# Performance work log

Measured on AMD Instinct MI355X. Metric: run time of the kernel, lower is better.

## Reference

```python
import jax, jax.numpy as jnp
import numpy as np

EPS = 1e-5  # torch GroupNorm default


def setup_inputs() -> dict:
    key = jax.random.key(0)
    k1, k2, k3 = jax.random.split(key, 3)
    bs, l, dim = 16, 2048, 512
    G, varDim, numCodes = 2, 256, 320
    x = jax.random.normal(k1, (bs, l, dim), dtype=jnp.float32)
    # grouped 1x1 Conv1d weight: (groups, out_per_group, in_per_group)
    proj_w = jax.random.normal(k2, (G, varDim, varDim), dtype=jnp.float32) / np.sqrt(varDim)
    gn_weight = jnp.ones((dim,), dtype=jnp.float32)
    gn_bias = jnp.zeros((dim,), dtype=jnp.float32)
    embeddings = 0.01 * jax.random.normal(k3, (numCodes, 1, varDim), dtype=jnp.float32)
    return {"x": x, "proj_w": proj_w, "gn_weight": gn_weight,
            "gn_bias": gn_bias, "embeddings": embeddings}


def reference(x, proj_w, gn_weight, gn_bias, embeddings):
    bs, l, dim = x.shape
    G, varDim, _ = proj_w.shape
    numCodes = embeddings.shape[0]

    # --- projection: grouped 1x1 conv ---
    xg = x.transpose(0, 2, 1).reshape(bs, G, varDim, l)            # (bs,G,v,l)
    ze_g = jnp.einsum('gov,bgvl->bgol', proj_w, xg)                # (bs,G,v,l)

    # --- Fp32GroupNorm over (C/G * L) per group ---
    zf = ze_g.astype(jnp.float32)
    mean = zf.mean(axis=(2, 3), keepdims=True)
    var = zf.var(axis=(2, 3), keepdims=True)
    zn = (zf - mean) * jax.lax.rsqrt(var + EPS)
    ze = zn.reshape(bs, dim, l) * gn_weight[None, :, None] + gn_bias[None, :, None]
    ze = ze.astype(x.dtype)                                        # (bs,dim,l)

    # --- VQ: nearest code per group (argmin of L2 == argmin of sq dist) ---
    z = ze.reshape(bs, G, varDim, l).transpose(0, 3, 1, 2)         # (bs,l,G,v)
    emb = jnp.broadcast_to(embeddings, (numCodes, G, varDim))      # combineGroups expand
    dots = jnp.einsum('blgv,cgv->blgc', z, emb)                    # (bs,l,G,C)
    e2 = jnp.sum(emb * emb, axis=-1)                               # (C,G)
    dist = e2.T[None, None] - 2.0 * dots                           # ||z||^2 dropped: const over C
    idx = jnp.argmin(dist, axis=-1)                                # (bs,l,G)

    # gather codes per group
    zq = jnp.take_along_axis(
        emb.transpose(1, 0, 2)[None, None],                        # (1,1,G,C,v)
        idx[..., None, None], axis=3).squeeze(3)                   # (bs,l,G,v)
    zq = zq.reshape(bs, l, dim)

    # straight-through estimator; output shape (bs, l, dim)
    ze_bld = ze.transpose(0, 2, 1)
    out = jax.lax.stop_gradient(zq) + ze_bld - jax.lax.stop_gradient(ze_bld)
    return out
```

## Files before the change

### kernel.cpp

```cpp
#include <hip/hip_runtime.h>
#include <math.h>

typedef _Float16 half8_t  __attribute__((ext_vector_type(8)));
typedef _Float16 half4_t  __attribute__((ext_vector_type(4)));
typedef float    floatx16 __attribute__((ext_vector_type(16)));

#define BS   16
#define LL   2048
#define DIMC 512
#define NG   2
#define VD   256
#define NC   320
#define NELEM ((double)(VD*LL))

__global__ void k_prep(const float* __restrict__ W, const float* __restrict__ emb,
                       _Float16* __restrict__ Whg, _Float16* __restrict__ Wlg,
                       _Float16* __restrict__ Ehg, _Float16* __restrict__ Elg)
{
  int id = blockIdx.x * 256 + threadIdx.x;
  if (id < NG * VD * VD) {
    float w = W[id] * 16.0f;
    _Float16 h = (_Float16)w;
    Whg[id] = h;
    Wlg[id] = (_Float16)(w - (float)h);
  } else {
    int j = id - NG * VD * VD;
    if (j < NC * VD) {
      float e = emb[j] * 64.0f;
      _Float16 h = (_Float16)e;
      Ehg[j] = h;
      Elg[j] = (_Float16)(e - (float)h);
    }
  }
}

__global__ __launch_bounds__(256, 2) void k_proj(
    const float* __restrict__ x,
    const _Float16* __restrict__ Whg, const _Float16* __restrict__ Wlg,
    float* __restrict__ ze, double* __restrict__ stats)
{
  __shared__ _Float16 Ah[128][72];
  __shared__ _Float16 Bh[128][72];

  const int blk = blockIdx.x;
  const int g  = blk & 1;
  const int nb = (blk >> 1) & 1;
  const int mt = blk >> 2;
  const int m0 = mt * 128;
  const int n0 = nb * 128;
  const int b  = m0 >> 11;
  const int t  = threadIdx.x;
  const int lane = t & 63;
  const int w    = t >> 6;
  const int col  = lane & 31;
  const int hq   = lane >> 5;
  const int mw   = (w & 1) * 64;
  const int nw   = (w >> 1) * 64;

  floatx16 acc[2][2];
  #pragma unroll
  for (int i = 0; i < 2; ++i)
    #pragma unroll
    for (int j = 0; j < 2; ++j)
      #pragma unroll
      for (int e = 0; e < 16; ++e) acc[i][j][e] = 0.f;

  for (int k0 = 0; k0 < VD; k0 += 32) {
    #pragma unroll
    for (int i = 0; i < 4; ++i) {
      int idx = i * 256 + t;
      int row = idx >> 3, kq = idx & 7;
      float4 v = *(const float4*)(x + ((size_t)(m0 + row)) * DIMC + g * VD + k0 + kq * 4);
      half4_t hh, ll;
      { _Float16 h = (_Float16)v.x; hh[0] = h; ll[0] = (_Float16)(v.x - (float)h); }
      { _Float16 h = (_Float16)v.y; hh[1] = h; ll[1] = (_Float16)(v.y - (float)h); }
      { _Float16 h = (_Float16)v.z; hh[2] = h; ll[2] = (_Float16)(v.z - (float)h); }
      { _Float16 h = (_Float16)v.w; hh[3] = h; ll[3] = (_Float16)(v.w - (float)h); }
      *(half4_t*)&Ah[row][kq * 4]      = hh;
      *(half4_t*)&Ah[row][32 + kq * 4] = ll;
    }
    #pragma unroll
    for (int i = 0; i < 2; ++i) {
      int idx = i * 256 + t;
      int row = idx >> 2, kc = idx & 3;
      size_t off = ((size_t)(g * VD + n0 + row)) * VD + k0 + kc * 8;
      *(half8_t*)&Bh[row][kc * 8]      = *(const half8_t*)(Whg + off);
      *(half8_t*)&Bh[row][32 + kc * 8] = *(const half8_t*)(Wlg + off);
    }
    __syncthreads();
    #pragma unroll
    for (int ks = 0; ks < 2; ++ks) {
      const int ko = ks * 16 + hq * 8;
      half8_t azh[2], azl[2], bwh[2], bwl[2];
      #pragma unroll
      for (int i2 = 0; i2 < 2; ++i2) {
        azh[i2] = *(const half8_t*)&Ah[mw + i2 * 32 + col][ko];
        azl[i2] = *(const half8_t*)&Ah[mw + i2 * 32 + col][32 + ko];
        bwh[i2] = *(const half8_t*)&Bh[nw + i2 * 32 + col][ko];
        bwl[i2] = *(const half8_t*)&Bh[nw + i2 * 32 + col][32 + ko];
      }
      #pragma unroll
      for (int mi = 0; mi < 2; ++mi)
        #pragma unroll
        for (int ni = 0; ni < 2; ++ni) {
          acc[mi][ni] = __builtin_amdgcn_mfma_f32_32x32x16_f16(azh[mi], bwh[ni], acc[mi][ni], 0, 0, 0);
          acc[mi][ni] = __builtin_amdgcn_mfma_f32_32x32x16_f16(azh[mi], bwl[ni], acc[mi][ni], 0, 0, 0);
          acc[mi][ni] = __builtin_amdgcn_mfma_f32_32x32x16_f16(azl[mi], bwh[ni], acc[mi][ni], 0, 0, 0);
        }
    }
    __syncthreads();
  }

  double s1 = 0.0, s2 = 0.0;
  #pragma unroll
  for (int mi = 0; mi < 2; ++mi)
    #pragma unroll
    for (int ni = 0; ni < 2; ++ni)
      #pragma unroll
      for (int r = 0; r < 16; ++r) {
        float vv = acc[mi][ni][r] * 0.0625f;
        double d = (double)vv; s1 += d; s2 += d * d;
        int ml = mw + mi * 32 + (r & 3) + 8 * (r >> 2) + 4 * hq;
        int nl = nw + ni * 32 + col;
        ze[((size_t)(m0 + ml)) * DIMC + g * VD + n0 + nl] = vv;
      }
  #pragma unroll
  for (int off = 32; off > 0; off >>= 1) {
    s1 += __shfl_down(s1, off);
    s2 += __shfl_down(s2, off);
  }
  if (lane == 0) {
    atomicAdd(&stats[(b * NG + g) * 2 + 0], s1);
    atomicAdd(&stats[(b * NG + g) * 2 + 1], s2);
  }
}

__global__ void k_fin(const double* __restrict__ stats,
                      const float* __restrict__ emb,
                      float* __restrict__ msr, float* __restrict__ e2f)
{
  const int t = threadIdx.x;
  if (blockIdx.x == 0) {
    if (t < BS * NG) {
      double s1 = stats[2 * t], s2 = stats[2 * t + 1];
      double mean = s1 / NELEM;
      double var  = s2 / NELEM - mean * mean;
      double rstd = 1.0 / sqrt(var + 1e-5);
      msr[t]      = (float)mean;
      msr[32 + t] = (float)rstd;
    }
  } else {
    const int c = (blockIdx.x - 1) * 64 + t;
    const float* er = emb + (size_t)c * VD;
    double s[4] = {0.0, 0.0, 0.0, 0.0};
    #pragma unroll
    for (int v = 0; v < VD; v += 16) {
      #pragma unroll
      for (int u = 0; u < 4; ++u) {
        float4 e4 = *(const float4*)(er + v + u * 4);
        s[u] += (double)e4.x * e4.x + (double)e4.y * e4.y
              + (double)e4.z * e4.z + (double)e4.w * e4.w;
      }
    }
    e2f[c] = (float)(64.0 * (s[0] + s[1] + s[2] + s[3]));
  }
}

__global__ __launch_bounds__(256, 2) void k_vq(
    float* __restrict__ zio, const float* __restrict__ emb,
    const _Float16* __restrict__ Ehg, const _Float16* __restrict__ Elg,
    const float* __restrict__ gnw, const float* __restrict__ gnb,
    const float* __restrict__ msr, const float* __restrict__ e2f)
{
  __shared__ _Float16 Ah[64][72];
  __shared__ _Float16 Es[320][72];
  __shared__ float e2sh[NC];
  __shared__ int idxs[64];

  const int blk = blockIdx.x;
  const int g  = blk & 1;
  const int m0 = (blk >> 1) * 64;
  const int b  = m0 >> 11;
  const int t  = threadIdx.x;
  const int lane = t & 63;
  const int w    = t >> 6;
  const int col  = lane & 31;
  const int hq   = lane >> 5;
  const int mhalf = w & 1;
  const int nhalf = w >> 1;
  const int ml = mhalf * 32 + col;

  const float mean = msr[b * NG + g];
  const float rstd = msr[32 + b * NG + g];
  for (int c = t; c < NC; c += 256) e2sh[c] = e2f[c];

  float* zbase = zio + ((size_t)m0) * DIMC + g * VD;
  const float* gw = gnw + g * VD;
  const float* gb = gnb + g * VD;

  floatx16 acc[5];
  #pragma unroll
  for (int i = 0; i < 5; ++i)
    #pragma unroll
    for (int e = 0; e < 16; ++e) acc[i][e] = 0.f;

  for (int k0 = 0; k0 < VD; k0 += 32) {
    #pragma unroll
    for (int i = 0; i < 2; ++i) {
      int idx = i * 256 + t;
      int row = idx >> 3, kq = idx & 7;
      float4 v  = *(const float4*)(zbase + ((size_t)row) * DIMC + k0 + kq * 4);
      float4 w4 = *(const float4*)(gw + k0 + kq * 4);
      float4 b4 = *(const float4*)(gb + k0 + kq * 4);
      float zn0 = (v.x - mean) * rstd * w4.x + b4.x;
      float zn1 = (v.y - mean) * rstd * w4.y + b4.y;
      float zn2 = (v.z - mean) * rstd * w4.z + b4.z;
      float zn3 = (v.w - mean) * rstd * w4.w + b4.w;
      half4_t hh, ll;
      { _Float16 h = (_Float16)zn0; hh[0] = h; ll[0] = (_Float16)(zn0 - (float)h); }
      { _Float16 h = (_Float16)zn1; hh[1] = h; ll[1] = (_Float16)(zn1 - (float)h); }
      { _Float16 h = (_Float16)zn2; hh[2] = h; ll[2] = (_Float16)(zn2 - (float)h); }
      { _Float16 h = (_Float16)zn3; hh[3] = h; ll[3] = (_Float16)(zn3 - (float)h); }
      *(half4_t*)&Ah[row][kq * 4]      = hh;
      *(half4_t*)&Ah[row][32 + kq * 4] = ll;
    }
    #pragma unroll
    for (int i = 0; i < 5; ++i) {
      int idx = i * 256 + t;
      int row = idx >> 2, kc = idx & 3;
      size_t off = ((size_t)row) * VD + k0 + kc * 8;
      *(half8_t*)&Es[row][kc * 8]      = *(const half8_t*)(Ehg + off);
      *(half8_t*)&Es[row][32 + kc * 8] = *(const half8_t*)(Elg + off);
    }
    __syncthreads();
    #pragma unroll
    for (int ks = 0; ks < 2; ++ks) {
      const int ko = ks * 16 + hq * 8;
      half8_t azh = *(const half8_t*)&Ah[ml][ko];
      half8_t azl = *(const half8_t*)&Ah[ml][32 + ko];
      #pragma unroll
      for (int nt = 0; nt < 5; ++nt) {
        int nr = nhalf * 160 + nt * 32 + col;
        half8_t beh = *(const half8_t*)&Es[nr][ko];
        half8_t bel = *(const half8_t*)&Es[nr][32 + ko];
        acc[nt] = __builtin_amdgcn_mfma_f32_32x32x16_f16(azh, beh, acc[nt], 0, 0, 0);
        acc[nt] = __builtin_amdgcn_mfma_f32_32x32x16_f16(azh, bel, acc[nt], 0, 0, 0);
        acc[nt] = __builtin_amdgcn_mfma_f32_32x32x16_f16(azl, beh, acc[nt], 0, 0, 0);
      }
    }
    __syncthreads();
  }

  float* bestv = (float*)&Es[0][0];
  int*   besti = (int*)((char*)&Es[0][0] + 64 * 65 * 4);
  #pragma unroll
  for (int r = 0; r < 16; ++r) {
    int mloc = mhalf * 32 + (r & 3) + 8 * (r >> 2) + 4 * hq;
    float bv = 3.4e38f; int bn = 0;
    #pragma unroll
    for (int nt = 0; nt < 5; ++nt) {
      int n = nhalf * 160 + nt * 32 + col;
      float d = e2sh[n] - 2.0f * acc[nt][r];
      if (d < bv) { bv = d; bn = n; }
    }
    bestv[mloc * 65 + nhalf * 32 + col] = bv;
    besti[mloc * 65 + nhalf * 32 + col] = bn;
  }
  __syncthreads();
  if (t < 64) {
    float bv = bestv[t * 65]; int bn = besti[t * 65];
    for (int j = 1; j < 64; ++j) {
      float v = bestv[t * 65 + j]; int n = besti[t * 65 + j];
      if (v < bv || (v == bv && n < bn)) { bv = v; bn = n; }
    }
    idxs[t] = bn;
  }
  __syncthreads();

  #pragma unroll
  for (int it = 0; it < 16; ++it) {
    int idx = it * 256 + t;
    int row = idx >> 6, q4 = (idx & 63) * 4;
    int id = idxs[row];
    float4 zr = *(const float4*)(zbase + (size_t)row * DIMC + q4);
    float4 w4 = *(const float4*)(gw + q4);
    float4 b4 = *(const float4*)(gb + q4);
    float4 e4 = *(const float4*)(emb + (size_t)id * VD + q4);
    float4 o; float zn;
    zn = (zr.x - mean) * rstd * w4.x + b4.x; o.x = (e4.x + zn) - zn;
    zn = (zr.y - mean) * rstd * w4.y + b4.y; o.y = (e4.y + zn) - zn;
    zn = (zr.z - mean) * rstd * w4.z + b4.z; o.z = (e4.z + zn) - zn;
    zn = (zr.w - mean) * rstd * w4.w + b4.w; o.w = (e4.w + zn) - zn;
    *(float4*)(zbase + (size_t)row * DIMC + q4) = o;
  }
}

extern "C" void kernel_launch(void* const* d_in, const int* in_sizes, int n_in,
                              void* d_out, int out_size, void* d_ws, size_t ws_size,
                              hipStream_t stream) {
  const float* x   = (const float*)d_in[0];
  const float* W   = (const float*)d_in[1];
  const float* gnw = (const float*)d_in[2];
  const float* gnb = (const float*)d_in[3];
  const float* emb = (const float*)d_in[4];
  float* out = (float*)d_out;

  double*   stats = (double*)d_ws;
  float*    msr   = (float*)((char*)d_ws + 512);
  float*    e2f   = (float*)((char*)d_ws + 768);
  _Float16* Whg   = (_Float16*)((char*)d_ws + 4096);
  _Float16* Wlg   = (_Float16*)((char*)d_ws + 266240);
  _Float16* Ehg   = (_Float16*)((char*)d_ws + 528384);
  _Float16* Elg   = (_Float16*)((char*)d_ws + 692224);

  hipMemsetAsync(d_ws, 0, 512, stream);
  k_prep<<<(NG * VD * VD + NC * VD + 255) / 256, 256, 0, stream>>>(W, emb, Whg, Wlg, Ehg, Elg);
  k_proj<<<1024, 256, 0, stream>>>(x, Whg, Wlg, out, stats);
  k_fin<<<6, 64, 0, stream>>>(stats, emb, msr, e2f);
  k_vq<<<1024, 256, 0, stream>>>(out, emb, Ehg, Elg, gnw, gnb, msr, e2f);
}
```

Before: 231.7 us.

## Widen GEMM tiles, prebuild LDS images, direct global-to-LDS loads, fold finalize kernel

```diff
diff --git a/kernel.cpp b/kernel.cpp
--- a/kernel.cpp
+++ b/kernel.cpp
@@ -13,64 +13,84 @@
 #define NC   320
 #define NELEM ((double)(VD*LL))
 
+#define GLL(gsrc, ldst) __builtin_amdgcn_global_load_lds( \
+    (const __attribute__((address_space(1))) unsigned int*)(gsrc), \
+    (__attribute__((address_space(3))) unsigned int*)(ldst), 16, 0, 0)
+
 __global__ void k_prep(const float* __restrict__ W, const float* __restrict__ emb,
-                       _Float16* __restrict__ Whg, _Float16* __restrict__ Wlg,
-                       _Float16* __restrict__ Ehg, _Float16* __restrict__ Elg)
+                       _Float16* __restrict__ Wimg, _Float16* __restrict__ Eimg,
+                       float* __restrict__ e2f, double* __restrict__ stats)
 {
-  int id = blockIdx.x * 256 + threadIdx.x;
-  if (id < NG * VD * VD) {
+  const int blk = blockIdx.x, t = threadIdx.x;
+  if (blk < 512) {
+    int id = blk * 256 + t;
+    int k = id & 255, c = k >> 5, kk = k & 31;
+    int row = (id >> 8) & 255, g = id >> 16;
     float w = W[id] * 16.0f;
     _Float16 h = (_Float16)w;
-    Whg[id] = h;
-    Wlg[id] = (_Float16)(w - (float)h);
+    size_t base = ((size_t)(g * 8 + c) * 256 + row) * 72;
+    Wimg[base + kk]      = h;
+    Wimg[base + 32 + kk] = (_Float16)(w - (float)h);
+  } else if (blk < 832) {
+    int j = (blk - 512) * 256 + t;
+    int k = j & 255, c = k >> 5, kk = k & 31;
+    int code = j >> 8;
+    float e = emb[j] * 64.0f;
+    _Float16 h = (_Float16)e;
+    size_t base = ((size_t)c * 320 + code) * 72;
+    Eimg[base + kk]      = h;
+    Eimg[base + 32 + kk] = (_Float16)(e - (float)h);
+  } else if (blk < 834) {
+    int code = (blk - 832) * 256 + t;
+    if (code < NC) {
+      const float* er = emb + (size_t)code * VD;
+      double s[4] = {0.0, 0.0, 0.0, 0.0};
+      for (int v = 0; v < VD; v += 16)
+        #pragma unroll
+        for (int u = 0; u < 4; ++u) {
+          float4 e4 = *(const float4*)(er + v + u * 4);
+          s[u] += (double)e4.x * e4.x + (double)e4.y * e4.y
+                + (double)e4.z * e4.z + (double)e4.w * e4.w;
+        }
+      e2f[code] = (float)(64.0 * (s[0] + s[1] + s[2] + s[3]));
+    }
   } else {
-    int j = id - NG * VD * VD;
-    if (j < NC * VD) {
-      float e = emb[j] * 64.0f;
-      _Float16 h = (_Float16)e;
-      Ehg[j] = h;
-      Elg[j] = (_Float16)(e - (float)h);
-    }
+    if (t < 64) stats[t] = 0.0;
   }
 }
 
 __global__ __launch_bounds__(256, 2) void k_proj(
-    const float* __restrict__ x,
-    const _Float16* __restrict__ Whg, const _Float16* __restrict__ Wlg,
+    const float* __restrict__ x, const _Float16* __restrict__ Wimg,
     float* __restrict__ ze, double* __restrict__ stats)
 {
   __shared__ _Float16 Ah[128][72];
-  __shared__ _Float16 Bh[128][72];
+  __shared__ _Float16 Bh[256 * 72];
 
   const int blk = blockIdx.x;
   const int g  = blk & 1;
-  const int nb = (blk >> 1) & 1;
-  const int mt = blk >> 2;
-  const int m0 = mt * 128;
-  const int n0 = nb * 128;
+  const int m0 = (blk >> 1) * 128;
   const int b  = m0 >> 11;
   const int t  = threadIdx.x;
-  const int lane = t & 63;
-  const int w    = t >> 6;
-  const int col  = lane & 31;
-  const int hq   = lane >> 5;
-  const int mw   = (w & 1) * 64;
-  const int nw   = (w >> 1) * 64;
-
-  floatx16 acc[2][2];
+  const int lane = t & 63, w = t >> 6;
+  const int col  = lane & 31, hq = lane >> 5;
+  const int mw = (w & 1) * 64, nw = (w >> 1) * 128;
+
+  const char* wbase = (const char*)(Wimg + (size_t)g * 8 * 256 * 72);
+
+  floatx16 acc[2][4];
   #pragma unroll
   for (int i = 0; i < 2; ++i)
     #pragma unroll
-    for (int j = 0; j < 2; ++j)
+    for (int j = 0; j < 4; ++j)
       #pragma unroll
       for (int e = 0; e < 16; ++e) acc[i][j][e] = 0.f;
 
-  for (int k0 = 0; k0 < VD; k0 += 32) {
+  for (int c = 0; c < 8; ++c) {
     #pragma unroll
     for (int i = 0; i < 4; ++i) {
       int idx = i * 256 + t;
       int row = idx >> 3, kq = idx & 7;
-      float4 v = *(const float4*)(x + ((size_t)(m0 + row)) * DIMC + g * VD + k0 + kq * 4);
+      float4 v = *(const float4*)(x + ((size_t)(m0 + row)) * DIMC + g * VD + c * 32 + kq * 4);
       half4_t hh, ll;
       { _Float16 h = (_Float16)v.x; hh[0] = h; ll[0] = (_Float16)(v.x - (float)h); }
       { _Float16 h = (_Float16)v.y; hh[1] = h; ll[1] = (_Float16)(v.y - (float)h); }
@@ -79,30 +99,33 @@
       *(half4_t*)&Ah[row][kq * 4]      = hh;
       *(half4_t*)&Ah[row][32 + kq * 4] = ll;
     }
-    #pragma unroll
-    for (int i = 0; i < 2; ++i) {
-      int idx = i * 256 + t;
-      int row = idx >> 2, kc = idx & 3;
-      size_t off = ((size_t)(g * VD + n0 + row)) * VD + k0 + kc * 8;
-      *(half8_t*)&Bh[row][kc * 8]      = *(const half8_t*)(Whg + off);
-      *(half8_t*)&Bh[row][32 + kc * 8] = *(const half8_t*)(Wlg + off);
+    {
+      const char* wc = wbase + (size_t)c * 256 * 144;
+      #pragma unroll
+      for (int i = 0; i < 9; ++i) {
+        int off = (w * 9 + i) * 1024 + lane * 16;
+        GLL(wc + off, (char*)Bh + off);
+      }
     }
     __syncthreads();
     #pragma unroll
     for (int ks = 0; ks < 2; ++ks) {
       const int ko = ks * 16 + hq * 8;
-      half8_t azh[2], azl[2], bwh[2], bwl[2];
-      #pragma unroll
-      for (int i2 = 0; i2 < 2; ++i2) {
-        azh[i2] = *(const half8_t*)&Ah[mw + i2 * 32 + col][ko];
-        azl[i2] = *(const half8_t*)&Ah[mw + i2 * 32 + col][32 + ko];
-        bwh[i2] = *(const half8_t*)&Bh[nw + i2 * 32 + col][ko];
-        bwl[i2] = *(const half8_t*)&Bh[nw + i2 * 32 + col][32 + ko];
+      half8_t azh[2], azl[2], bwh[4], bwl[4];
+      #pragma unroll
+      for (int i = 0; i < 2; ++i) {
+        azh[i] = *(const half8_t*)&Ah[mw + i * 32 + col][ko];
+        azl[i] = *(const half8_t*)&Ah[mw + i * 32 + col][32 + ko];
+      }
+      #pragma unroll
+      for (int j = 0; j < 4; ++j) {
+        bwh[j] = *(const half8_t*)&Bh[(nw + j * 32 + col) * 72 + ko];
+        bwl[j] = *(const half8_t*)&Bh[(nw + j * 32 + col) * 72 + 32 + ko];
       }
       #pragma unroll
       for (int mi = 0; mi < 2; ++mi)
         #pragma unroll
-        for (int ni = 0; ni < 2; ++ni) {
+        for (int ni = 0; ni < 4; ++ni) {
           acc[mi][ni] = __builtin_amdgcn_mfma_f32_32x32x16_f16(azh[mi], bwh[ni], acc[mi][ni], 0, 0, 0);
           acc[mi][ni] = __builtin_amdgcn_mfma_f32_32x32x16_f16(azh[mi], bwl[ni], acc[mi][ni], 0, 0, 0);
           acc[mi][ni] = __builtin_amdgcn_mfma_f32_32x32x16_f16(azl[mi], bwh[ni], acc[mi][ni], 0, 0, 0);
@@ -115,14 +138,14 @@
   #pragma unroll
   for (int mi = 0; mi < 2; ++mi)
     #pragma unroll
-    for (int ni = 0; ni < 2; ++ni)
+    for (int ni = 0; ni < 4; ++ni)
       #pragma unroll
       for (int r = 0; r < 16; ++r) {
         float vv = acc[mi][ni][r] * 0.0625f;
         double d = (double)vv; s1 += d; s2 += d * d;
         int ml = mw + mi * 32 + (r & 3) + 8 * (r >> 2) + 4 * hq;
         int nl = nw + ni * 32 + col;
-        ze[((size_t)(m0 + ml)) * DIMC + g * VD + n0 + nl] = vv;
+        ze[((size_t)(m0 + ml)) * DIMC + g * VD + nl] = vv;
       }
   #pragma unroll
   for (int off = 32; off > 0; off >>= 1) {
@@ -135,83 +158,51 @@
   }
 }
 
-__global__ void k_fin(const double* __restrict__ stats,
-                      const float* __restrict__ emb,
-                      float* __restrict__ msr, float* __restrict__ e2f)
-{
-  const int t = threadIdx.x;
-  if (blockIdx.x == 0) {
-    if (t < BS * NG) {
-      double s1 = stats[2 * t], s2 = stats[2 * t + 1];
-      double mean = s1 / NELEM;
-      double var  = s2 / NELEM - mean * mean;
-      double rstd = 1.0 / sqrt(var + 1e-5);
-      msr[t]      = (float)mean;
-      msr[32 + t] = (float)rstd;
-    }
-  } else {
-    const int c = (blockIdx.x - 1) * 64 + t;
-    const float* er = emb + (size_t)c * VD;
-    double s[4] = {0.0, 0.0, 0.0, 0.0};
-    #pragma unroll
-    for (int v = 0; v < VD; v += 16) {
-      #pragma unroll
-      for (int u = 0; u < 4; ++u) {
-        float4 e4 = *(const float4*)(er + v + u * 4);
-        s[u] += (double)e4.x * e4.x + (double)e4.y * e4.y
-              + (double)e4.z * e4.z + (double)e4.w * e4.w;
-      }
-    }
-    e2f[c] = (float)(64.0 * (s[0] + s[1] + s[2] + s[3]));
-  }
-}
-
 __global__ __launch_bounds__(256, 2) void k_vq(
     float* __restrict__ zio, const float* __restrict__ emb,
-    const _Float16* __restrict__ Ehg, const _Float16* __restrict__ Elg,
+    const _Float16* __restrict__ Eimg,
     const float* __restrict__ gnw, const float* __restrict__ gnb,
-    const float* __restrict__ msr, const float* __restrict__ e2f)
+    const double* __restrict__ stats, const float* __restrict__ e2f)
 {
-  __shared__ _Float16 Ah[64][72];
-  __shared__ _Float16 Es[320][72];
+  __shared__ _Float16 Zs[128][72];
+  __shared__ _Float16 Es[320 * 72];
   __shared__ float e2sh[NC];
-  __shared__ int idxs[64];
+  __shared__ int idxs[128];
 
   const int blk = blockIdx.x;
   const int g  = blk & 1;
-  const int m0 = (blk >> 1) * 64;
+  const int m0 = (blk >> 1) * 128;
   const int b  = m0 >> 11;
   const int t  = threadIdx.x;
-  const int lane = t & 63;
-  const int w    = t >> 6;
-  const int col  = lane & 31;
-  const int hq   = lane >> 5;
-  const int mhalf = w & 1;
-  const int nhalf = w >> 1;
-  const int ml = mhalf * 32 + col;
-
-  const float mean = msr[b * NG + g];
-  const float rstd = msr[32 + b * NG + g];
+  const int lane = t & 63, w = t >> 6;
+  const int col  = lane & 31, hq = lane >> 5;
+
+  const int si = b * NG + g;
+  double ss1 = stats[2 * si], ss2 = stats[2 * si + 1];
+  double mu = ss1 / NELEM, var = ss2 / NELEM - mu * mu;
+  const float mean = (float)mu;
+  const float rstd = (float)(1.0 / sqrt(var + 1e-5));
+
   for (int c = t; c < NC; c += 256) e2sh[c] = e2f[c];
 
-  float* zbase = zio + ((size_t)m0) * DIMC + g * VD;
+  float* zbase = zio + (size_t)m0 * DIMC + g * VD;
   const float* gw = gnw + g * VD;
   const float* gb = gnb + g * VD;
 
-  floatx16 acc[5];
-  #pragma unroll
-  for (int i = 0; i < 5; ++i)
+  floatx16 acc[10];
+  #pragma unroll
+  for (int i = 0; i < 10; ++i)
     #pragma unroll
     for (int e = 0; e < 16; ++e) acc[i][e] = 0.f;
 
-  for (int k0 = 0; k0 < VD; k0 += 32) {
-    #pragma unroll
-    for (int i = 0; i < 2; ++i) {
+  for (int c = 0; c < 8; ++c) {
+    #pragma unroll
+    for (int i = 0; i < 4; ++i) {
       int idx = i * 256 + t;
       int row = idx >> 3, kq = idx & 7;
-      float4 v  = *(const float4*)(zbase + ((size_t)row) * DIMC + k0 + kq * 4);
-      float4 w4 = *(const float4*)(gw + k0 + kq * 4);
-      float4 b4 = *(const float4*)(gb + k0 + kq * 4);
+      float4 v  = *(const float4*)(zbase + (size_t)row * DIMC + c * 32 + kq * 4);
+      float4 w4 = *(const float4*)(gw + c * 32 + kq * 4);
+      float4 b4 = *(const float4*)(gb + c * 32 + kq * 4);
       float zn0 = (v.x - mean) * rstd * w4.x + b4.x;
       float zn1 = (v.y - mean) * rstd * w4.y + b4.y;
       float zn2 = (v.z - mean) * rstd * w4.z + b4.z;
@@ -221,64 +212,53 @@
       { _Float16 h = (_Float16)zn1; hh[1] = h; ll[1] = (_Float16)(zn1 - (float)h); }
       { _Float16 h = (_Float16)zn2; hh[2] = h; ll[2] = (_Float16)(zn2 - (float)h); }
       { _Float16 h = (_Float16)zn3; hh[3] = h; ll[3] = (_Float16)(zn3 - (float)h); }
-      *(half4_t*)&Ah[row][kq * 4]      = hh;
-      *(half4_t*)&Ah[row][32 + kq * 4] = ll;
-    }
-    #pragma unroll
-    for (int i = 0; i < 5; ++i) {
-      int idx = i * 256 + t;
-      int row = idx >> 2, kc = idx & 3;
-      size_t off = ((size_t)row) * VD + k0 + kc * 8;
-      *(half8_t*)&Es[row][kc * 8]      = *(const half8_t*)(Ehg + off);
-      *(half8_t*)&Es[row][32 + kc * 8] = *(const half8_t*)(Elg + off);
+      *(half4_t*)&Zs[row][kq * 4]      = hh;
+      *(half4_t*)&Zs[row][32 + kq * 4] = ll;
+    }
+    {
+      const char* ec = (const char*)Eimg + (size_t)c * 320 * 144;
+      for (int i = w; i < 45; i += 4) {
+        int off = i * 1024 + lane * 16;
+        GLL(ec + off, (char*)Es + off);
+      }
     }
     __syncthreads();
     #pragma unroll
     for (int ks = 0; ks < 2; ++ks) {
       const int ko = ks * 16 + hq * 8;
-      half8_t azh = *(const half8_t*)&Ah[ml][ko];
-      half8_t azl = *(const half8_t*)&Ah[ml][32 + ko];
-      #pragma unroll
-      for (int nt = 0; nt < 5; ++nt) {
-        int nr = nhalf * 160 + nt * 32 + col;
-        half8_t beh = *(const half8_t*)&Es[nr][ko];
-        half8_t bel = *(const half8_t*)&Es[nr][32 + ko];
-        acc[nt] = __builtin_amdgcn_mfma_f32_32x32x16_f16(azh, beh, acc[nt], 0, 0, 0);
-        acc[nt] = __builtin_amdgcn_mfma_f32_32x32x16_f16(azh, bel, acc[nt], 0, 0, 0);
-        acc[nt] = __builtin_amdgcn_mfma_f32_32x32x16_f16(azl, beh, acc[nt], 0, 0, 0);
-      }
-    }
-    __syncthreads();
-  }
-
-  float* bestv = (float*)&Es[0][0];
-  int*   besti = (int*)((char*)&Es[0][0] + 64 * 65 * 4);
-  #pragma unroll
-  for (int r = 0; r < 16; ++r) {
-    int mloc = mhalf * 32 + (r & 3) + 8 * (r >> 2) + 4 * hq;
-    float bv = 3.4e38f; int bn = 0;
-    #pragma unroll
-    for (int nt = 0; nt < 5; ++nt) {
-      int n = nhalf * 160 + nt * 32 + col;
-      float d = e2sh[n] - 2.0f * acc[nt][r];
-      if (d < bv) { bv = d; bn = n; }
-    }
-    bestv[mloc * 65 + nhalf * 32 + col] = bv;
-    besti[mloc * 65 + nhalf * 32 + col] = bn;
-  }
+      half8_t bzh = *(const half8_t*)&Zs[w * 32 + col][ko];
+      half8_t bzl = *(const half8_t*)&Zs[w * 32 + col][32 + ko];
+      #pragma unroll
+      for (int mt = 0; mt < 10; ++mt) {
+        half8_t aeh = *(const half8_t*)&Es[(mt * 32 + col) * 72 + ko];
+        half8_t ael = *(const half8_t*)&Es[(mt * 32 + col) * 72 + 32 + ko];
+        acc[mt] = __builtin_amdgcn_mfma_f32_32x32x16_f16(aeh, bzh, acc[mt], 0, 0, 0);
+        acc[mt] = __builtin_amdgcn_mfma_f32_32x32x16_f16(aeh, bzl, acc[mt], 0, 0, 0);
+        acc[mt] = __builtin_amdgcn_mfma_f32_32x32x16_f16(ael, bzh, acc[mt], 0, 0, 0);
+      }
+    }
+    __syncthreads();
+  }
+
+  float bv = 3.4e38f; int bi = 0x7fffffff;
+  #pragma unroll
+  for (int mt = 0; mt < 10; ++mt)
+    #pragma unroll
+    for (int r = 0; r < 16; ++r) {
+      int code = mt * 32 + (r & 3) + 8 * (r >> 2) + 4 * hq;
+      float d = e2sh[code] - 2.0f * acc[mt][r];
+      if (d < bv || (d == bv && code < bi)) { bv = d; bi = code; }
+    }
+  {
+    float ov = __shfl_xor(bv, 32);
+    int   oi = __shfl_xor(bi, 32);
+    if (ov < bv || (ov == bv && oi < bi)) { bv = ov; bi = oi; }
+  }
+  if (hq == 0) idxs[w * 32 + col] = bi;
   __syncthreads();
-  if (t < 64) {
-    float bv = bestv[t * 65]; int bn = besti[t * 65];
-    for (int j = 1; j < 64; ++j) {
-      float v = bestv[t * 65 + j]; int n = besti[t * 65 + j];
-      if (v < bv || (v == bv && n < bn)) { bv = v; bn = n; }
-    }
-    idxs[t] = bn;
-  }
-  __syncthreads();
-
-  #pragma unroll
-  for (int it = 0; it < 16; ++it) {
+
+  #pragma unroll
+  for (int it = 0; it < 32; ++it) {
     int idx = it * 256 + t;
     int row = idx >> 6, q4 = (idx & 63) * 4;
     int id = idxs[row];
@@ -306,16 +286,11 @@
   float* out = (float*)d_out;
 
   double*   stats = (double*)d_ws;
-  float*    msr   = (float*)((char*)d_ws + 512);
-  float*    e2f   = (float*)((char*)d_ws + 768);
-  _Float16* Whg   = (_Float16*)((char*)d_ws + 4096);
-  _Float16* Wlg   = (_Float16*)((char*)d_ws + 266240);
-  _Float16* Ehg   = (_Float16*)((char*)d_ws + 528384);
-  _Float16* Elg   = (_Float16*)((char*)d_ws + 692224);
-
-  hipMemsetAsync(d_ws, 0, 512, stream);
-  k_prep<<<(NG * VD * VD + NC * VD + 255) / 256, 256, 0, stream>>>(W, emb, Whg, Wlg, Ehg, Elg);
-  k_proj<<<1024, 256, 0, stream>>>(x, Whg, Wlg, out, stats);
-  k_fin<<<6, 64, 0, stream>>>(stats, emb, msr, e2f);
-  k_vq<<<1024, 256, 0, stream>>>(out, emb, Ehg, Elg, gnw, gnb, msr, e2f);
-}
+  float*    e2f   = (float*)((char*)d_ws + 512);
+  _Float16* Wimg  = (_Float16*)((char*)d_ws + 2048);
+  _Float16* Eimg  = (_Float16*)((char*)d_ws + 591872);
+
+  k_prep<<<835, 256, 0, stream>>>(W, emb, Wimg, Eimg, e2f, stats);
+  k_proj<<<512, 256, 0, stream>>>(x, Wimg, out, stats);
+  k_vq<<<512, 256, 0, stream>>>(out, emb, Eimg, gnw, gnb, stats, e2f);
+}
```

After: 208.1 us. 10.2% less time.
